# Kernel optimization log

Hardware: AMD Instinct MI355X
Metric: run time of the kernel (lower is better)

The kernel has to match this reference:

```python
import jax, jax.numpy as jnp
import numpy as np

B, S, D = 4, 2048, 1024
H, DK = 16, 64
NEG = -1e9


def setup_inputs() -> dict:
    key = jax.random.key(0)
    ks = jax.random.split(key, 6)
    hidden_states = jax.random.normal(ks[0], (B, S, D), dtype=jnp.float32)
    # evidence-constrained mask: causal mask plus random evidence restriction
    causal = jnp.tril(jnp.ones((S, S), dtype=bool))
    evid = jax.random.bernoulli(ks[1], 0.7, (S, S))
    allowed = causal & (evid | jnp.eye(S, dtype=bool))  # diag always allowed
    attention_mask = jnp.where(allowed, 0.0, NEG).astype(jnp.float32)
    scale = 0.02
    Wq = jax.random.normal(ks[2], (H * DK, D), dtype=jnp.float32) * scale
    Wk = jax.random.normal(ks[3], (H * DK, D), dtype=jnp.float32) * scale
    Wv = jax.random.normal(ks[4], (H * DK, D), dtype=jnp.float32) * scale
    Wo = jax.random.normal(ks[5], (D, H * DK), dtype=jnp.float32) * scale
    return {"hidden_states": hidden_states, "attention_mask": attention_mask,
            "Wq": Wq, "Wk": Wk, "Wv": Wv, "Wo": Wo}


def reference(hidden_states, attention_mask, Wq, Wk, Wv, Wo):
    b, s, _ = hidden_states.shape
    # nn.Linear(bias=False): y = x @ W.T ; reshape to (B,H,S,DK)
    def proj(x, W):
        y = jnp.einsum('bsd,ed->bse', x, W)
        return y.reshape(b, s, H, DK).transpose(0, 2, 1, 3)
    q = proj(hidden_states, Wq)
    k = proj(hidden_states, Wk)
    v = proj(hidden_states, Wv)
    logits = jnp.einsum('bhqd,bhkd->bhqk', q, k) / jnp.sqrt(jnp.float32(DK))
    logits = logits + attention_mask[None, None, :, :]
    attn = jax.nn.softmax(logits, axis=-1)
    ctx = jnp.einsum('bhqk,bhkd->bhqd', attn, v)
    ctx = ctx.transpose(0, 2, 1, 3).reshape(b, s, H * DK)
    out = jnp.einsum('bse,de->bsd', ctx, Wo)
    return out
```

## Files before the change

kernel.cpp:

```cpp
#include <hip/hip_runtime.h>
#include <hip/hip_bf16.h>
#include <math.h>

#define B_  4
#define S_  2048
#define D_  1024
#define H_  16
#define DK_ 64
#define M_  (B_*S_)
#define E_  (H_*DK_)
#define LOG2E  1.4426950408889634f
#define QSCALE 0.18033688011112042f

typedef short  bf16x8 __attribute__((ext_vector_type(8)));
typedef float  f32x4  __attribute__((ext_vector_type(4)));
typedef unsigned short u16;
typedef unsigned int   u32;
typedef unsigned long long u64;

__device__ __forceinline__ u16 f2b(float x) {
    __hip_bfloat16 h = __float2bfloat16(x);
    return *(u16*)&h;
}

__device__ __forceinline__ u32 cvtpk(float lo, float hi) {
    u32 r;
    asm("v_cvt_pk_bf16_f32 %0, %1, %2" : "=v"(r) : "v"(lo), "v"(hi));
    return r;
}

__device__ __forceinline__ void async16(const u16* g, u16* l) {
    __builtin_amdgcn_global_load_lds(
        (const __attribute__((address_space(1))) unsigned int*)g,
        (__attribute__((address_space(3))) unsigned int*)l, 16, 0, 0);
}

#define XN8 (M_ * D_ / 8)
#define WN8 (E_ * D_ / 8)
__global__ __launch_bounds__(256)
void cvt_all(const float* __restrict__ X,
             const float* __restrict__ Wq, const float* __restrict__ Wk,
             const float* __restrict__ Wv, const float* __restrict__ Wo,
             u16* __restrict__ Xb,
             u16* __restrict__ Wqb, u16* __restrict__ Wkb,
             u16* __restrict__ Wvb, u16* __restrict__ Wob) {
    int idx = blockIdx.x * 256 + threadIdx.x;
    const float* s; u16* d; int off;
    if (idx < XN8) { s = X; d = Xb; off = idx; }
    else {
        int j = idx - XN8;
        int which = j / WN8; off = j - which * WN8;
        s = which == 0 ? Wq : which == 1 ? Wk : which == 2 ? Wv : Wo;
        d = which == 0 ? Wqb : which == 1 ? Wkb : which == 2 ? Wvb : Wob;
    }
    const float4* s4 = (const float4*)s;
    float4 a = s4[2 * off], b = s4[2 * off + 1];
    u16 o[8] = {f2b(a.x), f2b(a.y), f2b(a.z), f2b(a.w),
                f2b(b.x), f2b(b.y), f2b(b.z), f2b(b.w)};
    *(uint4*)(d + (size_t)8 * off) = *(const uint4*)o;
}

__global__ __launch_bounds__(256)
void maskcvt(const float* __restrict__ mask, u32* __restrict__ bits) {
    const int w   = threadIdx.x >> 6;
    const int lane = threadIdx.x & 63;
    const int row = blockIdx.x * 4 + w;
    const float* mr = mask + (size_t)row * S_;
    u64* br = (u64*)(bits + (size_t)row * (S_ / 32));
    #pragma unroll
    for (int i = 0; i < S_ / 64; i++) {
        float v = mr[i * 64 + lane];
        u64 bal = __ballot(v == 0.0f);
        if (lane == 0) br[i] = bal;
    }
}

__device__ __forceinline__ void gemm_core(
    const u16* __restrict__ Ag, const u16* __restrict__ Bg, int K,
    int bm, int bn, u16* As, u16* Bs, f32x4 (&acc)[4][4])
{
    const int tid  = threadIdx.x;
    const int w    = tid >> 6, lane = tid & 63;
    const int l15  = lane & 15, quad = lane >> 4;
    const int wm   = (w >> 1) * 64, wn = (w & 1) * 64;
    const int srow = lane >> 3;
    const int sg   = (lane & 7) ^ srow;
    const int sx   = l15 & 7;

    for (int k0 = 0; k0 < K; k0 += 64) {
        __syncthreads();
        #pragma unroll
        for (int i = 0; i < 4; i++) {
            const int row = w * 32 + i * 8 + srow;
            async16(Ag + (size_t)(bm + row) * K + k0 + sg * 8,
                    As + (size_t)(w * 32 + i * 8) * 64);
            async16(Bg + (size_t)(bn + row) * K + k0 + sg * 8,
                    Bs + (size_t)(w * 32 + i * 8) * 64);
        }
        __syncthreads();

        #pragma unroll
        for (int s = 0; s < 2; s++) {
            bf16x8 af[4], bf[4];
            #pragma unroll
            for (int i = 0; i < 4; i++)
                af[i] = *(const bf16x8*)(As + (size_t)(wm + i * 16 + l15) * 64
                                            + (((s * 4 + quad) ^ sx) * 8));
            #pragma unroll
            for (int j = 0; j < 4; j++)
                bf[j] = *(const bf16x8*)(Bs + (size_t)(wn + j * 16 + l15) * 64
                                            + (((s * 4 + quad) ^ sx) * 8));
            #pragma unroll
            for (int i = 0; i < 4; i++)
                #pragma unroll
                for (int j = 0; j < 4; j++)
                    acc[i][j] = __builtin_amdgcn_mfma_f32_16x16x32_bf16(af[i], bf[j], acc[i][j], 0, 0, 0);
        }
    }
}

__global__ __launch_bounds__(256)
void gemm_qkv(const u16* __restrict__ Xb,
              const u16* __restrict__ Wqb, const u16* __restrict__ Wkb,
              const u16* __restrict__ Wvb,
              u16* __restrict__ Qm, u16* __restrict__ Km, u16* __restrict__ Vt)
{
    __shared__ u16 As[128 * 64];
    __shared__ u16 Bs[128 * 64];
    const int bm    = blockIdx.x * 128;
    const int nb    = blockIdx.y;
    const int which = nb >> 3;
    const int col0  = (nb & 7) * 128;
    const u16* Bg = which == 0 ? Wqb : which == 1 ? Wkb : Wvb;

    f32x4 acc[4][4] = {};
    gemm_core(Xb, Bg, D_, bm, col0, As, Bs, acc);

    const int tid = threadIdx.x;
    const int w   = tid >> 6, lane = tid & 63;
    const int l15 = lane & 15, quad = lane >> 4;
    const int wm  = (w >> 1) * 64, wn = (w & 1) * 64;

    if (which == 2) {
        #pragma unroll
        for (int i = 0; i < 4; i++)
            #pragma unroll
            for (int j = 0; j < 4; j++) {
                int c    = col0 + wn + j * 16 + l15;
                int tok0 = bm + wm + i * 16 + quad * 4;
                int u    = tok0 & 63;
                int perm = (u & 32) | ((u & 12) << 1) | ((u & 16) >> 2);
                int tp   = (tok0 & (2047 & ~63)) | perm;
                u16 pk[4] = {f2b(acc[i][j][0]), f2b(acc[i][j][1]),
                             f2b(acc[i][j][2]), f2b(acc[i][j][3])};
                size_t idx = (((size_t)((tok0 >> 11) * E_ + c)) << 11) + tp;
                *(uint2*)(Vt + idx) = *(const uint2*)pk;
            }
    } else {
        u16* Cm = which == 0 ? Qm : Km;
        const float sc = which == 0 ? QSCALE : 1.0f;
        #pragma unroll
        for (int i = 0; i < 4; i++)
            #pragma unroll
            for (int j = 0; j < 4; j++)
                #pragma unroll
                for (int r = 0; r < 4; r++) {
                    int row = bm + wm + i * 16 + quad * 4 + r;
                    int c   = col0 + wn + j * 16 + l15;
                    Cm[(size_t)row * E_ + c] = f2b(acc[i][j][r] * sc);
                }
    }
}

__global__ __launch_bounds__(256)
void gemm_out(const u16* __restrict__ Cmx, const u16* __restrict__ Wob,
              float* __restrict__ out)
{
    __shared__ u16 As[128 * 64];
    __shared__ u16 Bs[128 * 64];
    const int bm = blockIdx.x * 128;
    const int bn = blockIdx.y * 128;

    f32x4 acc[4][4] = {};
    gemm_core(Cmx, Wob, E_, bm, bn, As, Bs, acc);

    const int tid = threadIdx.x;
    const int w   = tid >> 6, lane = tid & 63;
    const int l15 = lane & 15, quad = lane >> 4;
    const int wm  = (w >> 1) * 64, wn = (w & 1) * 64;
    #pragma unroll
    for (int i = 0; i < 4; i++)
        #pragma unroll
        for (int j = 0; j < 4; j++)
            #pragma unroll
            for (int r = 0; r < 4; r++)
                out[(size_t)(bm + wm + i * 16 + quad * 4 + r) * D_ + bn + wn + j * 16 + l15]
                    = acc[i][j][r];
}

__global__ __launch_bounds__(512, 4)
void flash_attn(const u16* __restrict__ Q, const u16* __restrict__ Kc,
                const u16* __restrict__ Vt, const u32* __restrict__ bits,
                u16* __restrict__ ctx)
{
    const int bh  = blockIdx.x;
    const int y   = blockIdx.y;
    const int qt  = (y < 4) ? (7 - y) : (y - 4);
    const int b   = bh >> 4, h = bh & 15;
    const int tid = threadIdx.x;
    const int w   = tid >> 6, lane = tid & 63;
    const int l15 = lane & 15, quad = lane >> 4;
    const int q0  = qt * 256;
    const int nkt = 4 * qt + 4;

    __shared__ u16 Ks[2][64 * 64];
    __shared__ u16 Vs[2][64 * 64];

    const u16* qbA = Q + ((size_t)(b * S_ + q0 + w * 32 + l15)) * E_ + h * DK_;
    bf16x8 qfA0 = *(const bf16x8*)(qbA + quad * 8);
    bf16x8 qfA1 = *(const bf16x8*)(qbA + 32 + quad * 8);
    const u16* qbB = qbA + (size_t)16 * E_;
    bf16x8 qfB0 = *(const bf16x8*)(qbB + quad * 8);
    bf16x8 qfB1 = *(const bf16x8*)(qbB + 32 + quad * 8);

    f32x4 accA[4] = {}, accB[4] = {};
    f32x4 accLA = {}, accLB = {};

    const int sr = lane >> 3;
    const int sg = (lane & 7) ^ sr;
    const int sx = l15 & 7;

    const u32* mrowA = bits + (size_t)(q0 + w * 32 + l15) * (S_ / 32);
    const u32* mrowB = mrowA + 16 * (S_ / 32);
    const u16* kg = Kc + ((size_t)(b * S_ + w * 8 + sr)) * E_ + h * DK_ + sg * 8;
    const u16* vg = Vt + ((size_t)(bh * DK_ + w * 8 + sr)) * S_ + sg * 8;

    async16(kg, &Ks[0][w * 512]); kg += (size_t)64 * E_;
    async16(vg, &Vs[0][w * 512]); vg += 64;
    u64 mwAn = *(const u64*)mrowA;
    u64 mwBn = *(const u64*)mrowB;

    union { u32 w4[4]; bf16x8 v; } ones;
    ones.w4[0] = ones.w4[1] = ones.w4[2] = ones.w4[3] = 0x3F803F80u;

    int cur = 0;
    for (int kt = 0; kt < nkt; ++kt) {
        const int nxt = cur ^ 1;
        __syncthreads();
        u64 mwA = mwAn, mwB = mwBn;
        if (kt + 1 < nkt) {
            async16(kg, &Ks[nxt][w * 512]); kg += (size_t)64 * E_;
            async16(vg, &Vs[nxt][w * 512]); vg += 64;
            mwAn = *(const u64*)(mrowA + ((kt + 1) << 1));
            mwBn = *(const u64*)(mrowB + ((kt + 1) << 1));
        }

        const u16* Kb = Ks[cur];
        const u16* Vb = Vs[cur];

        #pragma unroll
        for (int sb = 0; sb < 2; sb++) {
            f32x4 stA[2] = {}, stB[2] = {};
            #pragma unroll
            for (int tt = 0; tt < 2; tt++) {
                const int t = 2 * sb + tt;
                bf16x8 kf0 = *(const bf16x8*)(Kb + (t * 16 + l15) * 64 + ((quad ^ sx) * 8));
                bf16x8 kf1 = *(const bf16x8*)(Kb + (t * 16 + l15) * 64 + (((4 + quad) ^ sx) * 8));
                stA[tt] = __builtin_amdgcn_mfma_f32_16x16x32_bf16(kf0, qfA0, stA[tt], 0, 0, 0);
                stA[tt] = __builtin_amdgcn_mfma_f32_16x16x32_bf16(kf1, qfA1, stA[tt], 0, 0, 0);
                stB[tt] = __builtin_amdgcn_mfma_f32_16x16x32_bf16(kf0, qfB0, stB[tt], 0, 0, 0);
                stB[tt] = __builtin_amdgcn_mfma_f32_16x16x32_bf16(kf1, qfB1, stB[tt], 0, 0, 0);
            }

            const u64 sA = mwA >> (quad * 4 + sb * 32);
            const u64 sB = mwB >> (quad * 4 + sb * 32);
            #pragma unroll
            for (int tt = 0; tt < 2; tt++) {
                const u32 nA = (u32)(sA >> (tt * 16)) & 0xF;
                const u32 nB = (u32)(sB >> (tt * 16)) & 0xF;
                stA[tt][0] = (nA & 1) ? exp2f(stA[tt][0]) : 0.0f;
                stA[tt][1] = (nA & 2) ? exp2f(stA[tt][1]) : 0.0f;
                stA[tt][2] = (nA & 4) ? exp2f(stA[tt][2]) : 0.0f;
                stA[tt][3] = (nA & 8) ? exp2f(stA[tt][3]) : 0.0f;
                stB[tt][0] = (nB & 1) ? exp2f(stB[tt][0]) : 0.0f;
                stB[tt][1] = (nB & 2) ? exp2f(stB[tt][1]) : 0.0f;
                stB[tt][2] = (nB & 4) ? exp2f(stB[tt][2]) : 0.0f;
                stB[tt][3] = (nB & 8) ? exp2f(stB[tt][3]) : 0.0f;
            }

            union { u32 w4[4]; bf16x8 v; } puA, puB;
            puA.w4[0] = cvtpk(stA[0][0], stA[0][1]);
            puA.w4[1] = cvtpk(stA[0][2], stA[0][3]);
            puA.w4[2] = cvtpk(stA[1][0], stA[1][1]);
            puA.w4[3] = cvtpk(stA[1][2], stA[1][3]);
            puB.w4[0] = cvtpk(stB[0][0], stB[0][1]);
            puB.w4[1] = cvtpk(stB[0][2], stB[0][3]);
            puB.w4[2] = cvtpk(stB[1][0], stB[1][1]);
            puB.w4[3] = cvtpk(stB[1][2], stB[1][3]);

            accLA = __builtin_amdgcn_mfma_f32_16x16x32_bf16(puA.v, ones.v, accLA, 0, 0, 0);
            accLB = __builtin_amdgcn_mfma_f32_16x16x32_bf16(puB.v, ones.v, accLB, 0, 0, 0);

            #pragma unroll
            for (int nt = 0; nt < 4; nt++) {
                bf16x8 vf = *(const bf16x8*)(Vb + (nt * 16 + l15) * 64
                                                + (((4 * sb + quad) ^ sx) * 8));
                accA[nt] = __builtin_amdgcn_mfma_f32_16x16x32_bf16(puA.v, vf, accA[nt], 0, 0, 0);
                accB[nt] = __builtin_amdgcn_mfma_f32_16x16x32_bf16(puB.v, vf, accB[nt], 0, 0, 0);
            }
        }
        cur = nxt;
    }

    #pragma unroll
    for (int r = 0; r < 4; r++) {
        float irA = 1.0f / accLA[r];
        float irB = 1.0f / accLB[r];
        size_t oA = ((size_t)(b * S_ + q0 + w * 32 + quad * 4 + r)) * E_ + h * DK_;
        size_t oB = oA + (size_t)16 * E_;
        #pragma unroll
        for (int nt = 0; nt < 4; nt++) {
            ctx[oA + nt * 16 + l15] = f2b(accA[nt][r] * irA);
            ctx[oB + nt * 16 + l15] = f2b(accB[nt][r] * irB);
        }
    }
}

extern "C" void kernel_launch(void* const* d_in, const int* in_sizes, int n_in,
                              void* d_out, int out_size, void* d_ws, size_t ws_size,
                              hipStream_t stream) {
    const float* X    = (const float*)d_in[0];
    const float* mask = (const float*)d_in[1];
    const float* Wq   = (const float*)d_in[2];
    const float* Wk   = (const float*)d_in[3];
    const float* Wv   = (const float*)d_in[4];
    const float* Wo   = (const float*)d_in[5];
    float* out = (float*)d_out;

    char* p = (char*)d_ws;
    u16* Qm  = (u16*)p; p += (size_t)M_ * E_ * 2;
    u16* Km  = (u16*)p; p += (size_t)M_ * E_ * 2;
    u16* Vt  = (u16*)p; p += (size_t)M_ * E_ * 2;
    u16* Wqb = (u16*)p; p += (size_t)E_ * D_ * 2;
    u16* Wkb = (u16*)p; p += (size_t)E_ * D_ * 2;
    u16* Wvb = (u16*)p; p += (size_t)E_ * D_ * 2;
    u16* Wob = (u16*)p; p += (size_t)D_ * E_ * 2;
    u32* Mb  = (u32*)p; p += (size_t)S_ * (S_ / 32) * 4;
    u16* Xb  = (u16*)p;
    u16* Cm  = Xb;

    cvt_all<<<(XN8 + 4 * WN8 + 255) / 256, 256, 0, stream>>>(
        X, Wq, Wk, Wv, Wo, Xb, Wqb, Wkb, Wvb, Wob);
    maskcvt<<<S_ / 4, 256, 0, stream>>>(mask, Mb);

    gemm_qkv<<<dim3(M_ / 128, 24), 256, 0, stream>>>(Xb, Wqb, Wkb, Wvb, Qm, Km, Vt);

    flash_attn<<<dim3(B_ * H_, S_ / 256), 512, 0, stream>>>(Qm, Km, Vt, Mb, Cm);

    gemm_out<<<dim3(M_ / 128, D_ / 128), 256, 0, stream>>>(Cm, Wob, out);
}
```

Measured before the change: 288.1 us.

## Halve attention query tile, merge mask conversion into cvt kernel, use native exp2

Changes the flash attention blocks from 512 threads covering 256 query rows to 256 threads covering 128 rows. The grid doubles and a new causal load-balancing order interleaves long and short tiles. Each wave now loads two 16-byte chunks of K and V per stage to fill the 64-row tile. The mask-to-bitmask conversion is folded into the cvt_all launch as extra blocks, removing one kernel launch. The exp2f calls are replaced with the native hardware exp2, trading some accuracy for fewer instructions.

```diff
diff --git a/kernel.cpp b/kernel.cpp
--- a/kernel.cpp
+++ b/kernel.cpp
@@ -18,6 +18,8 @@
 typedef unsigned int   u32;
 typedef unsigned long long u64;
 
+extern "C" __device__ float __ocml_native_exp2_f32(float);
+
 __device__ __forceinline__ u16 f2b(float x) {
     __hip_bfloat16 h = __float2bfloat16(x);
     return *(u16*)&h;
@@ -37,13 +39,30 @@
 
 #define XN8 (M_ * D_ / 8)
 #define WN8 (E_ * D_ / 8)
+#define CVTB ((XN8 + 4 * WN8) / 256)
 __global__ __launch_bounds__(256)
 void cvt_all(const float* __restrict__ X,
              const float* __restrict__ Wq, const float* __restrict__ Wk,
              const float* __restrict__ Wv, const float* __restrict__ Wo,
+             const float* __restrict__ mask,
              u16* __restrict__ Xb,
              u16* __restrict__ Wqb, u16* __restrict__ Wkb,
-             u16* __restrict__ Wvb, u16* __restrict__ Wob) {
+             u16* __restrict__ Wvb, u16* __restrict__ Wob,
+             u32* __restrict__ bits) {
+    if (blockIdx.x >= CVTB) {
+        const int w    = threadIdx.x >> 6;
+        const int lane = threadIdx.x & 63;
+        const int row  = (blockIdx.x - CVTB) * 4 + w;
+        const float* mr = mask + (size_t)row * S_;
+        u64* br = (u64*)(bits + (size_t)row * (S_ / 32));
+        #pragma unroll
+        for (int i = 0; i < S_ / 64; i++) {
+            float v = mr[i * 64 + lane];
+            u64 bal = __ballot(v == 0.0f);
+            if (lane == 0) br[i] = bal;
+        }
+        return;
+    }
     int idx = blockIdx.x * 256 + threadIdx.x;
     const float* s; u16* d; int off;
     if (idx < XN8) { s = X; d = Xb; off = idx; }
@@ -58,21 +77,6 @@
     u16 o[8] = {f2b(a.x), f2b(a.y), f2b(a.z), f2b(a.w),
                 f2b(b.x), f2b(b.y), f2b(b.z), f2b(b.w)};
     *(uint4*)(d + (size_t)8 * off) = *(const uint4*)o;
-}
-
-__global__ __launch_bounds__(256)
-void maskcvt(const float* __restrict__ mask, u32* __restrict__ bits) {
-    const int w   = threadIdx.x >> 6;
-    const int lane = threadIdx.x & 63;
-    const int row = blockIdx.x * 4 + w;
-    const float* mr = mask + (size_t)row * S_;
-    u64* br = (u64*)(bits + (size_t)row * (S_ / 32));
-    #pragma unroll
-    for (int i = 0; i < S_ / 64; i++) {
-        float v = mr[i * 64 + lane];
-        u64 bal = __ballot(v == 0.0f);
-        if (lane == 0) br[i] = bal;
-    }
 }
 
 __device__ __forceinline__ void gemm_core(
@@ -198,20 +202,21 @@
                     = acc[i][j][r];
 }
 
-__global__ __launch_bounds__(512, 4)
+__global__ __launch_bounds__(256, 2)
 void flash_attn(const u16* __restrict__ Q, const u16* __restrict__ Kc,
                 const u16* __restrict__ Vt, const u32* __restrict__ bits,
                 u16* __restrict__ ctx)
 {
     const int bh  = blockIdx.x;
     const int y   = blockIdx.y;
-    const int qt  = (y < 4) ? (7 - y) : (y - 4);
+    const int g   = y >> 2, r4 = y & 3;
+    const int qt  = g == 0 ? 15 - r4 : g == 1 ? r4 : g == 2 ? 11 - r4 : 4 + r4;
     const int b   = bh >> 4, h = bh & 15;
     const int tid = threadIdx.x;
     const int w   = tid >> 6, lane = tid & 63;
     const int l15 = lane & 15, quad = lane >> 4;
-    const int q0  = qt * 256;
-    const int nkt = 4 * qt + 4;
+    const int q0  = qt * 128;
+    const int nkt = 2 * qt + 2;
 
     __shared__ u16 Ks[2][64 * 64];
     __shared__ u16 Vs[2][64 * 64];
@@ -219,9 +224,8 @@
     const u16* qbA = Q + ((size_t)(b * S_ + q0 + w * 32 + l15)) * E_ + h * DK_;
     bf16x8 qfA0 = *(const bf16x8*)(qbA + quad * 8);
     bf16x8 qfA1 = *(const bf16x8*)(qbA + 32 + quad * 8);
-    const u16* qbB = qbA + (size_t)16 * E_;
-    bf16x8 qfB0 = *(const bf16x8*)(qbB + quad * 8);
-    bf16x8 qfB1 = *(const bf16x8*)(qbB + 32 + quad * 8);
+    bf16x8 qfB0 = *(const bf16x8*)(qbA + (size_t)16 * E_ + quad * 8);
+    bf16x8 qfB1 = *(const bf16x8*)(qbA + (size_t)16 * E_ + 32 + quad * 8);
 
     f32x4 accA[4] = {}, accB[4] = {};
     f32x4 accLA = {}, accLB = {};
@@ -232,11 +236,14 @@
 
     const u32* mrowA = bits + (size_t)(q0 + w * 32 + l15) * (S_ / 32);
     const u32* mrowB = mrowA + 16 * (S_ / 32);
-    const u16* kg = Kc + ((size_t)(b * S_ + w * 8 + sr)) * E_ + h * DK_ + sg * 8;
-    const u16* vg = Vt + ((size_t)(bh * DK_ + w * 8 + sr)) * S_ + sg * 8;
-
-    async16(kg, &Ks[0][w * 512]); kg += (size_t)64 * E_;
-    async16(vg, &Vs[0][w * 512]); vg += 64;
+    const u16* kg = Kc + ((size_t)(b * S_ + w * 16 + sr)) * E_ + h * DK_ + sg * 8;
+    const u16* vg = Vt + ((size_t)(bh * DK_ + w * 16 + sr)) * S_ + sg * 8;
+
+    async16(kg,                    &Ks[0][(w * 16) * 64]);
+    async16(kg + (size_t)8 * E_,   &Ks[0][(w * 16 + 8) * 64]);
+    async16(vg,                    &Vs[0][(w * 16) * 64]);
+    async16(vg + (size_t)8 * S_,   &Vs[0][(w * 16 + 8) * 64]);
+    kg += (size_t)64 * E_; vg += 64;
     u64 mwAn = *(const u64*)mrowA;
     u64 mwBn = *(const u64*)mrowB;
 
@@ -249,8 +256,11 @@
         __syncthreads();
         u64 mwA = mwAn, mwB = mwBn;
         if (kt + 1 < nkt) {
-            async16(kg, &Ks[nxt][w * 512]); kg += (size_t)64 * E_;
-            async16(vg, &Vs[nxt][w * 512]); vg += 64;
+            async16(kg,                  &Ks[nxt][(w * 16) * 64]);
+            async16(kg + (size_t)8 * E_, &Ks[nxt][(w * 16 + 8) * 64]);
+            async16(vg,                  &Vs[nxt][(w * 16) * 64]);
+            async16(vg + (size_t)8 * S_, &Vs[nxt][(w * 16 + 8) * 64]);
+            kg += (size_t)64 * E_; vg += 64;
             mwAn = *(const u64*)(mrowA + ((kt + 1) << 1));
             mwBn = *(const u64*)(mrowB + ((kt + 1) << 1));
         }
@@ -278,14 +288,14 @@
             for (int tt = 0; tt < 2; tt++) {
                 const u32 nA = (u32)(sA >> (tt * 16)) & 0xF;
                 const u32 nB = (u32)(sB >> (tt * 16)) & 0xF;
-                stA[tt][0] = (nA & 1) ? exp2f(stA[tt][0]) : 0.0f;
-                stA[tt][1] = (nA & 2) ? exp2f(stA[tt][1]) : 0.0f;
-                stA[tt][2] = (nA & 4) ? exp2f(stA[tt][2]) : 0.0f;
-                stA[tt][3] = (nA & 8) ? exp2f(stA[tt][3]) : 0.0f;
-                stB[tt][0] = (nB & 1) ? exp2f(stB[tt][0]) : 0.0f;
-                stB[tt][1] = (nB & 2) ? exp2f(stB[tt][1]) : 0.0f;
-                stB[tt][2] = (nB & 4) ? exp2f(stB[tt][2]) : 0.0f;
-                stB[tt][3] = (nB & 8) ? exp2f(stB[tt][3]) : 0.0f;
+                stA[tt][0] = (nA & 1) ? __ocml_native_exp2_f32(stA[tt][0]) : 0.0f;
+                stA[tt][1] = (nA & 2) ? __ocml_native_exp2_f32(stA[tt][1]) : 0.0f;
+                stA[tt][2] = (nA & 4) ? __ocml_native_exp2_f32(stA[tt][2]) : 0.0f;
+                stA[tt][3] = (nA & 8) ? __ocml_native_exp2_f32(stA[tt][3]) : 0.0f;
+                stB[tt][0] = (nB & 1) ? __ocml_native_exp2_f32(stB[tt][0]) : 0.0f;
+                stB[tt][1] = (nB & 2) ? __ocml_native_exp2_f32(stB[tt][1]) : 0.0f;
+                stB[tt][2] = (nB & 4) ? __ocml_native_exp2_f32(stB[tt][2]) : 0.0f;
+                stB[tt][3] = (nB & 8) ? __ocml_native_exp2_f32(stB[tt][3]) : 0.0f;
             }
 
             union { u32 w4[4]; bf16x8 v; } puA, puB;
@@ -349,13 +359,12 @@
     u16* Xb  = (u16*)p;
     u16* Cm  = Xb;
 
-    cvt_all<<<(XN8 + 4 * WN8 + 255) / 256, 256, 0, stream>>>(
-        X, Wq, Wk, Wv, Wo, Xb, Wqb, Wkb, Wvb, Wob);
-    maskcvt<<<S_ / 4, 256, 0, stream>>>(mask, Mb);
+    cvt_all<<<CVTB + 512, 256, 0, stream>>>(
+        X, Wq, Wk, Wv, Wo, mask, Xb, Wqb, Wkb, Wvb, Wob, Mb);
 
     gemm_qkv<<<dim3(M_ / 128, 24), 256, 0, stream>>>(Xb, Wqb, Wkb, Wvb, Qm, Km, Vt);
 
-    flash_attn<<<dim3(B_ * H_, S_ / 256), 512, 0, stream>>>(Qm, Km, Vt, Mb, Cm);
+    flash_attn<<<dim3(B_ * H_, S_ / 128), 256, 0, stream>>>(Qm, Km, Vt, Mb, Cm);
 
     gemm_out<<<dim3(M_ / 128, D_ / 128), 256, 0, stream>>>(Cm, Wob, out);
 }
```

Result: faster. 260.3 us (median of 2 runs) (-9.6%).
